# Performance work log

Measured on AMD Instinct MI355X. Metric: run time of the kernel, lower is better.

The kernel has to match this reference:

```python
import jax, jax.numpy as jnp
import numpy as np

R = 16
ALPHA = 16.0
SCALE = ALPHA / max(1, R)  # alpha / max(1, r)


def setup_inputs() -> dict:
    key = jax.random.key(0)
    k1, k2, k3, k4, k5 = jax.random.split(key, 5)
    B, S, D_IN, D_OUT = 4, 4096, 4096, 4096
    x = jax.random.normal(k1, (B, S, D_IN), dtype=jnp.float32)
    weight = jax.random.normal(k2, (D_OUT, D_IN), dtype=jnp.float32) * (1.0 / np.sqrt(D_IN))
    bias = jax.random.normal(k3, (D_OUT,), dtype=jnp.float32)
    lora_A = jax.random.normal(k4, (R, D_IN), dtype=jnp.float32) * (1.0 / np.sqrt(D_IN))
    lora_B = jax.random.normal(k5, (D_OUT, R), dtype=jnp.float32) * (1.0 / np.sqrt(R))
    return {"x": x, "weight": weight, "bias": bias, "lora_A": lora_A, "lora_B": lora_B}


def reference(x, weight, bias, lora_A, lora_B):
    # base = F.linear(x, weight, bias) = x @ W^T + b
    base = jnp.einsum('bsi,oi->bso', x, weight) + bias
    # lora = x @ (B @ A)^T = (x @ A^T) @ B^T  (chained low-rank, same math)
    xa = jnp.einsum('bsi,ri->bsr', x, lora_A)   # [B,S,r]
    lora = jnp.einsum('bsr,or->bso', xa, lora_B)  # [B,S,out]
    return base + SCALE * lora
```

## Files before the change

kernel.cpp:

```cpp
#include <hip/hip_runtime.h>
#include <hip/hip_bf16.h>
#include <stdint.h>

#define M_DIM 16384
#define N_DIM 4096
#define K_DIM 4096
#define LORA_SCALE 1.0f

typedef _Float16 half8 __attribute__((ext_vector_type(8)));
typedef float f32x4 __attribute__((ext_vector_type(4)));

__global__ __launch_bounds__(256) void cvt_x_kernel(const float* __restrict__ x,
                                                    _Float16* __restrict__ xb) {
    size_t base = ((size_t)blockIdx.x * 256 + (size_t)threadIdx.x) * 8;
    f32x4 a = *(const f32x4*)(x + base);
    f32x4 b = *(const f32x4*)(x + base + 4);
    half8 h;
    h[0] = (_Float16)a[0]; h[1] = (_Float16)a[1];
    h[2] = (_Float16)a[2]; h[3] = (_Float16)a[3];
    h[4] = (_Float16)b[0]; h[5] = (_Float16)b[1];
    h[6] = (_Float16)b[2]; h[7] = (_Float16)b[3];
    *(half8*)(xb + base) = h;
}

__global__ __launch_bounds__(256) void prep_w_kernel(const float* __restrict__ W,
                                                     const float* __restrict__ lA,
                                                     const float* __restrict__ lB,
                                                     _Float16* __restrict__ wp) {
    __shared__ float A_lds[16][256];
    __shared__ float B_lds[256];
    const int t = threadIdx.x;
    const int n0 = blockIdx.x * 16;

    B_lds[t] = lB[(size_t)n0 * 16 + t];

    for (int kc = 0; kc < 16; ++kc) {
        const int k = kc * 256 + t;
        __syncthreads();
#pragma unroll
        for (int r = 0; r < 16; ++r) A_lds[r][t] = lA[(size_t)r * K_DIM + k];
        __syncthreads();
#pragma unroll 4
        for (int row = 0; row < 16; ++row) {
            float acc = W[(size_t)(n0 + row) * K_DIM + k];
            float dot = 0.f;
#pragma unroll
            for (int r = 0; r < 16; ++r) dot += B_lds[row * 16 + r] * A_lds[r][t];
            acc += LORA_SCALE * dot;
            wp[(size_t)(n0 + row) * K_DIM + k] = (_Float16)acc;
        }
    }
}

__device__ inline void load_lds16(const void* g, void* l) {
    __builtin_amdgcn_global_load_lds(
        (const __attribute__((address_space(1))) unsigned int*)(uintptr_t)g,
        (__attribute__((address_space(3))) unsigned int*)(uintptr_t)l,
        16, 0, 0);
}

__global__ __launch_bounds__(256) void gemm_bt_kernel(const _Float16* __restrict__ A,
                                                      const _Float16* __restrict__ B,
                                                      const float* __restrict__ bias,
                                                      float* __restrict__ C) {
    __shared__ _Float16 As[128 * 32];
    __shared__ _Float16 Bs[128 * 32];

    const int tid  = threadIdx.x;
    const int lane = tid & 63;
    const int wave = tid >> 6;
    const int quad = lane >> 4;
    const int r16  = lane & 15;
    const int wm   = wave >> 1;
    const int wn   = wave & 1;

    const int m0 = blockIdx.y * 128;
    const int n0 = blockIdx.x * 128;

    const int c0 = tid;
    const int c1 = tid + 256;

    const _Float16* gA0 = A + (size_t)(m0 + (c0 >> 2)) * K_DIM + ((c0 & 3) << 3);
    const _Float16* gA1 = A + (size_t)(m0 + (c1 >> 2)) * K_DIM + ((c1 & 3) << 3);
    const _Float16* gB0 = B + (size_t)(n0 + (c0 >> 2)) * K_DIM + ((c0 & 3) << 3);
    const _Float16* gB1 = B + (size_t)(n0 + (c1 >> 2)) * K_DIM + ((c1 & 3) << 3);
    _Float16* lA0 = &As[c0 * 8];
    _Float16* lA1 = &As[c1 * 8];
    _Float16* lB0 = &Bs[c0 * 8];
    _Float16* lB1 = &Bs[c1 * 8];

    f32x4 acc[4][4] = {};

    for (int kt = 0; kt < K_DIM / 32; ++kt) {
        load_lds16(gA0, lA0);
        load_lds16(gA1, lA1);
        load_lds16(gB0, lB0);
        load_lds16(gB1, lB1);
        gA0 += 32; gA1 += 32; gB0 += 32; gB1 += 32;

        __syncthreads();

        half8 af[4], bf[4];
#pragma unroll
        for (int i = 0; i < 4; ++i)
            af[i] = *(const half8*)&As[(wm * 64 + i * 16 + r16) * 32 + quad * 8];
#pragma unroll
        for (int j = 0; j < 4; ++j)
            bf[j] = *(const half8*)&Bs[(wn * 64 + j * 16 + r16) * 32 + quad * 8];

#pragma unroll
        for (int i = 0; i < 4; ++i)
#pragma unroll
            for (int j = 0; j < 4; ++j)
                acc[i][j] = __builtin_amdgcn_mfma_f32_16x16x32_f16(af[i], bf[j],
                                                                   acc[i][j], 0, 0, 0);

        __syncthreads();
    }

#pragma unroll
    for (int j = 0; j < 4; ++j) {
        const int n = n0 + wn * 64 + j * 16 + r16;
        const float bv = bias[n];
#pragma unroll
        for (int i = 0; i < 4; ++i) {
            const int mbase = m0 + wm * 64 + i * 16 + quad * 4;
#pragma unroll
            for (int r = 0; r < 4; ++r) {
                C[(size_t)(mbase + r) * N_DIM + n] = acc[i][j][r] + bv;
            }
        }
    }
}

extern "C" void kernel_launch(void* const* d_in, const int* in_sizes, int n_in,
                              void* d_out, int out_size, void* d_ws, size_t ws_size,
                              hipStream_t stream) {
    const float* x      = (const float*)d_in[0];
    const float* weight = (const float*)d_in[1];
    const float* bias   = (const float*)d_in[2];
    const float* lora_A = (const float*)d_in[3];
    const float* lora_B = (const float*)d_in[4];
    float* out = (float*)d_out;

    _Float16* xb = (_Float16*)d_ws;
    _Float16* wp = (_Float16*)((char*)d_ws + (size_t)M_DIM * K_DIM * 2);

    cvt_x_kernel<<<dim3((M_DIM * (size_t)K_DIM) / (256 * 8)), dim3(256), 0, stream>>>(x, xb);
    prep_w_kernel<<<dim3(N_DIM / 16), dim3(256), 0, stream>>>(weight, lora_A, lora_B, wp);
    gemm_bt_kernel<<<dim3(N_DIM / 128, M_DIM / 128), dim3(256), 0, stream>>>(xb, wp, bias, out);
}
```

Before: 1.142 ms.

## Double GEMM K-tile to 64 with XOR-swizzled LDS and merge prep kernels

Raises the GEMM K tile from 32 to 64, so each iteration issues twice the MFMAs per pair of barriers. An XOR swizzle on the LDS column chunks is meant to avoid bank conflicts on the half8 fragment reads. The x-conversion and weight-prep kernels are merged into one launch, removing a launch and letting the two phases overlap. LDS use doubles to 32KB per block, which may reduce occupancy.

```diff
diff --git a/kernel.cpp b/kernel.cpp
--- a/kernel.cpp
+++ b/kernel.cpp
@@ -6,32 +6,36 @@
 #define N_DIM 4096
 #define K_DIM 4096
 #define LORA_SCALE 1.0f
+#define BK 64
+#define CVT_BLOCKS (M_DIM * K_DIM / 2048)
 
 typedef _Float16 half8 __attribute__((ext_vector_type(8)));
 typedef float f32x4 __attribute__((ext_vector_type(4)));
 
-__global__ __launch_bounds__(256) void cvt_x_kernel(const float* __restrict__ x,
-                                                    _Float16* __restrict__ xb) {
-    size_t base = ((size_t)blockIdx.x * 256 + (size_t)threadIdx.x) * 8;
-    f32x4 a = *(const f32x4*)(x + base);
-    f32x4 b = *(const f32x4*)(x + base + 4);
-    half8 h;
-    h[0] = (_Float16)a[0]; h[1] = (_Float16)a[1];
-    h[2] = (_Float16)a[2]; h[3] = (_Float16)a[3];
-    h[4] = (_Float16)b[0]; h[5] = (_Float16)b[1];
-    h[6] = (_Float16)b[2]; h[7] = (_Float16)b[3];
-    *(half8*)(xb + base) = h;
-}
-
-__global__ __launch_bounds__(256) void prep_w_kernel(const float* __restrict__ W,
-                                                     const float* __restrict__ lA,
-                                                     const float* __restrict__ lB,
-                                                     _Float16* __restrict__ wp) {
+__global__ __launch_bounds__(256) void pre_kernel(const float* __restrict__ x,
+                                                  const float* __restrict__ W,
+                                                  const float* __restrict__ lA,
+                                                  const float* __restrict__ lB,
+                                                  _Float16* __restrict__ xb,
+                                                  _Float16* __restrict__ wp) {
     __shared__ float A_lds[16][256];
     __shared__ float B_lds[256];
     const int t = threadIdx.x;
-    const int n0 = blockIdx.x * 16;
 
+    if (blockIdx.x < CVT_BLOCKS) {
+        size_t base = ((size_t)blockIdx.x * 256 + (size_t)t) * 8;
+        f32x4 a = *(const f32x4*)(x + base);
+        f32x4 b = *(const f32x4*)(x + base + 4);
+        half8 h;
+        h[0] = (_Float16)a[0]; h[1] = (_Float16)a[1];
+        h[2] = (_Float16)a[2]; h[3] = (_Float16)a[3];
+        h[4] = (_Float16)b[0]; h[5] = (_Float16)b[1];
+        h[6] = (_Float16)b[2]; h[7] = (_Float16)b[3];
+        *(half8*)(xb + base) = h;
+        return;
+    }
+
+    const int n0 = (blockIdx.x - CVT_BLOCKS) * 16;
     B_lds[t] = lB[(size_t)n0 * 16 + t];
 
     for (int kc = 0; kc < 16; ++kc) {
@@ -46,8 +50,7 @@
             float dot = 0.f;
 #pragma unroll
             for (int r = 0; r < 16; ++r) dot += B_lds[row * 16 + r] * A_lds[r][t];
-            acc += LORA_SCALE * dot;
-            wp[(size_t)(n0 + row) * K_DIM + k] = (_Float16)acc;
+            wp[(size_t)(n0 + row) * K_DIM + k] = (_Float16)(acc + LORA_SCALE * dot);
         }
     }
 }
@@ -63,57 +66,69 @@
                                                       const _Float16* __restrict__ B,
                                                       const float* __restrict__ bias,
                                                       float* __restrict__ C) {
-    __shared__ _Float16 As[128 * 32];
-    __shared__ _Float16 Bs[128 * 32];
+    __shared__ _Float16 As[128 * BK];
+    __shared__ _Float16 Bs[128 * BK];
 
     const int tid  = threadIdx.x;
     const int lane = tid & 63;
-    const int wave = tid >> 6;
     const int quad = lane >> 4;
     const int r16  = lane & 15;
+    const int wave = tid >> 6;
     const int wm   = wave >> 1;
     const int wn   = wave & 1;
 
     const int m0 = blockIdx.y * 128;
     const int n0 = blockIdx.x * 128;
 
-    const int c0 = tid;
-    const int c1 = tid + 256;
-
-    const _Float16* gA0 = A + (size_t)(m0 + (c0 >> 2)) * K_DIM + ((c0 & 3) << 3);
-    const _Float16* gA1 = A + (size_t)(m0 + (c1 >> 2)) * K_DIM + ((c1 & 3) << 3);
-    const _Float16* gB0 = B + (size_t)(n0 + (c0 >> 2)) * K_DIM + ((c0 & 3) << 3);
-    const _Float16* gB1 = B + (size_t)(n0 + (c1 >> 2)) * K_DIM + ((c1 & 3) << 3);
-    _Float16* lA0 = &As[c0 * 8];
-    _Float16* lA1 = &As[c1 * 8];
-    _Float16* lB0 = &Bs[c0 * 8];
-    _Float16* lB1 = &Bs[c1 * 8];
+    const _Float16* gA[4];
+    const _Float16* gB[4];
+    _Float16* lA[4];
+    _Float16* lB[4];
+#pragma unroll
+    for (int p = 0; p < 4; ++p) {
+        const int c    = tid + 256 * p;
+        const int row  = c >> 3;
+        const int colc = (c & 7) ^ (row & 7);
+        gA[p] = A + (size_t)(m0 + row) * K_DIM + colc * 8;
+        gB[p] = B + (size_t)(n0 + row) * K_DIM + colc * 8;
+        lA[p] = &As[c * 8];
+        lB[p] = &Bs[c * 8];
+    }
 
     f32x4 acc[4][4] = {};
 
-    for (int kt = 0; kt < K_DIM / 32; ++kt) {
-        load_lds16(gA0, lA0);
-        load_lds16(gA1, lA1);
-        load_lds16(gB0, lB0);
-        load_lds16(gB1, lB1);
-        gA0 += 32; gA1 += 32; gB0 += 32; gB1 += 32;
+    for (int kt = 0; kt < K_DIM / BK; ++kt) {
+#pragma unroll
+        for (int p = 0; p < 4; ++p) load_lds16(gA[p], lA[p]);
+#pragma unroll
+        for (int p = 0; p < 4; ++p) load_lds16(gB[p], lB[p]);
+#pragma unroll
+        for (int p = 0; p < 4; ++p) { gA[p] += BK; gB[p] += BK; }
 
         __syncthreads();
 
-        half8 af[4], bf[4];
 #pragma unroll
-        for (int i = 0; i < 4; ++i)
-            af[i] = *(const half8*)&As[(wm * 64 + i * 16 + r16) * 32 + quad * 8];
+        for (int s = 0; s < 2; ++s) {
+            half8 af[4], bf[4];
 #pragma unroll
-        for (int j = 0; j < 4; ++j)
-            bf[j] = *(const half8*)&Bs[(wn * 64 + j * 16 + r16) * 32 + quad * 8];
-
+            for (int i = 0; i < 4; ++i) {
+                const int row = wm * 64 + i * 16 + r16;
+                const int cc  = (s * 4 + quad) ^ (r16 & 7);
+                af[i] = *(const half8*)&As[row * BK + cc * 8];
+            }
 #pragma unroll
-        for (int i = 0; i < 4; ++i)
+            for (int j = 0; j < 4; ++j) {
+                const int row = wn * 64 + j * 16 + r16;
+                const int cc  = (s * 4 + quad) ^ (r16 & 7);
+                bf[j] = *(const half8*)&Bs[row * BK + cc * 8];
+            }
 #pragma unroll
-            for (int j = 0; j < 4; ++j)
-                acc[i][j] = __builtin_amdgcn_mfma_f32_16x16x32_f16(af[i], bf[j],
-                                                                   acc[i][j], 0, 0, 0);
+            for (int i = 0; i < 4; ++i)
+#pragma unroll
+                for (int j = 0; j < 4; ++j)
+                    acc[i][j] = __builtin_amdgcn_mfma_f32_16x16x32_f16(af[i], bf[j],
+                                                                       acc[i][j], 0, 0, 0);
+        }
 
         __syncthreads();
     }
@@ -146,7 +161,8 @@
     _Float16* xb = (_Float16*)d_ws;
     _Float16* wp = (_Float16*)((char*)d_ws + (size_t)M_DIM * K_DIM * 2);
 
-    cvt_x_kernel<<<dim3((M_DIM * (size_t)K_DIM) / (256 * 8)), dim3(256), 0, stream>>>(x, xb);
-    prep_w_kernel<<<dim3(N_DIM / 16), dim3(256), 0, stream>>>(weight, lora_A, lora_B, wp);
-    gemm_bt_kernel<<<dim3(N_DIM / 128, M_DIM / 128), dim3(256), 0, stream>>>(xb, wp, bias, out);
+    pre_kernel<<<dim3(CVT_BLOCKS + N_DIM / 16), dim3(256), 0, stream>>>(
+        x, weight, lora_A, lora_B, xb, wp);
+    gemm_bt_kernel<<<dim3(N_DIM / 128, M_DIM / 128), dim3(256), 0, stream>>>(
+        xb, wp, bias, out);
 }
```

New measurement: 1.170 ms. 2.5% more time.
